# Performance work log

Hardware: AMD Instinct MI355X
Metric: run time of the kernel (lower is better)

Reference implementation:

```python
import jax, jax.numpy as jnp
import numpy as np

B, K, D = 4, 8192, 1024


def setup_inputs() -> dict:
    key = jax.random.key(0)
    kx, kw, kb = jax.random.split(key, 3)
    x = jax.random.normal(kx, (B, K, D), dtype=jnp.float32)
    # torch.nn.Linear default init: U(-1/sqrt(fan_in), 1/sqrt(fan_in))
    bound = 1.0 / np.sqrt(D)
    W = jax.random.uniform(kw, (D, D), dtype=jnp.float32, minval=-bound, maxval=bound)
    b = jax.random.uniform(kb, (D,), dtype=jnp.float32, minval=-bound, maxval=bound)
    return {"x": x, "W": W, "b": b}


def reference(x, W, b):
    # lam_t = sigmoid(x_t @ W^T + b): compute for all timesteps in one GEMM
    lam = jax.nn.sigmoid(jnp.einsum("bkd,ed->bke", x, W) + b)  # [B,K,D]
    u_gated = (1.0 - lam) * x  # [B,K,D]

    def step(s, inputs):
        lam_t, ug_t = inputs  # each [B,D]
        s = lam_t * s + ug_t
        return s, s

    s0 = jnp.zeros((x.shape[0], x.shape[2]), dtype=x.dtype)
    # scan over time axis: move K to leading dim
    _, ys = jax.lax.scan(step, s0, (jnp.swapaxes(lam, 0, 1), jnp.swapaxes(u_gated, 0, 1)))
    return jnp.swapaxes(ys, 0, 1)  # [B,K,D]
```

## Files before the change

### kernel.cpp

```cpp
#include <hip/hip_runtime.h>
#include <hip/hip_bf16.h>
#include <cstdint>
#include <cstddef>

#define B_ 4
#define K_ 8192
#define D_ 1024
#define M_ (B_*K_)

#define CCH 256
#define LCH (K_/CCH)

typedef __bf16 bf16x8 __attribute__((ext_vector_type(8)));
typedef float  f32x4  __attribute__((ext_vector_type(4)));

typedef __attribute__((address_space(1))) void as1void;
typedef __attribute__((address_space(3))) void as3void;

__device__ __forceinline__ void gload_lds16(const void* g, void* l) {
  __builtin_amdgcn_global_load_lds((as1void*)g, (as3void*)l, 16, 0, 0);
}

__device__ __forceinline__ unsigned short f2bf_rne(float f) {
  unsigned u = __builtin_bit_cast(unsigned, f);
  u += 0x7fffu + ((u >> 16) & 1u);
  return (unsigned short)(u >> 16);
}

__global__ __launch_bounds__(256) void cvt_f32_to_bf16(
    const float* __restrict__ in, unsigned short* __restrict__ out, int n4) {
  int stride = gridDim.x * blockDim.x;
  for (int i = blockIdx.x * blockDim.x + threadIdx.x; i < n4; i += stride) {
    float4 v = reinterpret_cast<const float4*>(in)[i];
    ushort4 o;
    o.x = f2bf_rne(v.x); o.y = f2bf_rne(v.y);
    o.z = f2bf_rne(v.z); o.w = f2bf_rne(v.w);
    reinterpret_cast<ushort4*>(out)[i] = o;
  }
}

__global__ __launch_bounds__(256) void gemm_bias_sigmoid(
    const unsigned short* __restrict__ A,
    const unsigned short* __restrict__ Bw,
    const float* __restrict__ bias,
    float* __restrict__ lam) {
  __shared__ __attribute__((aligned(16))) unsigned short Alds[128 * 32];
  __shared__ __attribute__((aligned(16))) unsigned short Blds[128 * 32];

  const int t    = threadIdx.x;
  const int wave = t >> 6;
  const int lane = t & 63;
  const int wr   = wave >> 1;
  const int wc   = wave & 1;
  const int m0   = blockIdx.x * 128;
  const int n0   = blockIdx.y * 128;

  f32x4 acc[4][4] = {};

  const int r0 = t >> 2;
  const int c0 = (t & 3) * 8;
  const unsigned short* gA0 = A  + (size_t)(m0 + r0)      * D_ + c0;
  const unsigned short* gA1 = A  + (size_t)(m0 + r0 + 64) * D_ + c0;
  const unsigned short* gB0 = Bw + (size_t)(n0 + r0)      * D_ + c0;
  const unsigned short* gB1 = Bw + (size_t)(n0 + r0 + 64) * D_ + c0;
  unsigned short* lA0 = Alds + (       wave * 64) * 8;
  unsigned short* lA1 = Alds + (256 +  wave * 64) * 8;
  unsigned short* lB0 = Blds + (       wave * 64) * 8;
  unsigned short* lB1 = Blds + (256 +  wave * 64) * 8;

  const int aoff = (wr * 64 + (lane & 15)) * 32 + ((lane >> 4) * 8);
  const int boff = (wc * 64 + (lane & 15)) * 32 + ((lane >> 4) * 8);

  for (int kt = 0; kt < D_; kt += 32) {
    gload_lds16(gA0 + kt, lA0);
    gload_lds16(gA1 + kt, lA1);
    gload_lds16(gB0 + kt, lB0);
    gload_lds16(gB1 + kt, lB1);
    __syncthreads();
    bf16x8 af[4], bf[4];
#pragma unroll
    for (int m = 0; m < 4; ++m)
      af[m] = *reinterpret_cast<const bf16x8*>(&Alds[aoff + m * 16 * 32]);
#pragma unroll
    for (int n = 0; n < 4; ++n)
      bf[n] = *reinterpret_cast<const bf16x8*>(&Blds[boff + n * 16 * 32]);
#pragma unroll
    for (int m = 0; m < 4; ++m)
#pragma unroll
      for (int n = 0; n < 4; ++n)
        acc[m][n] = __builtin_amdgcn_mfma_f32_16x16x32_bf16(af[m], bf[n], acc[m][n], 0, 0, 0);
    __syncthreads();
  }

  const int erow = m0 + wr * 64 + ((lane >> 4) << 2);
  const int ecol = n0 + wc * 64 + (lane & 15);
#pragma unroll
  for (int n = 0; n < 4; ++n) {
    const int col = ecol + n * 16;
    const float bv = bias[col];
#pragma unroll
    for (int m = 0; m < 4; ++m) {
#pragma unroll
      for (int r = 0; r < 4; ++r) {
        const int row = erow + m * 16 + r;
        const float z = acc[m][n][r] + bv;
        lam[(size_t)row * D_ + col] = 1.0f / (1.0f + __expf(-z));
      }
    }
  }
}

__global__ __launch_bounds__(256) void scan_pass1(
    const float* __restrict__ lam, const float* __restrict__ x,
    float* __restrict__ P, float* __restrict__ Aarr) {
  const int blk = blockIdx.x;
  const int b = blk / CCH, c = blk % CCH;
  const int d4 = threadIdx.x * 4;
  const size_t base = ((size_t)(b * K_ + c * LCH)) * D_ + d4;
  const float4* lp = reinterpret_cast<const float4*>(lam + base);
  const float4* xp = reinterpret_cast<const float4*>(x + base);
  float4 s = {0.f, 0.f, 0.f, 0.f};
  float4 p = {1.f, 1.f, 1.f, 1.f};
#pragma unroll 8
  for (int k = 0; k < LCH; ++k) {
    float4 l  = lp[k * (D_ / 4)];
    float4 xv = xp[k * (D_ / 4)];
    p.x *= l.x; p.y *= l.y; p.z *= l.z; p.w *= l.w;
    s.x = l.x * s.x + (1.f - l.x) * xv.x;
    s.y = l.y * s.y + (1.f - l.y) * xv.y;
    s.z = l.z * s.z + (1.f - l.z) * xv.z;
    s.w = l.w * s.w + (1.f - l.w) * xv.w;
  }
  const size_t o = ((size_t)(b * CCH + c)) * D_ + d4;
  *reinterpret_cast<float4*>(P + o)    = p;
  *reinterpret_cast<float4*>(Aarr + o) = s;
}

__global__ __launch_bounds__(256) void scan_pass2(
    const float* __restrict__ P, const float* __restrict__ Aarr,
    float* __restrict__ S) {
  const int g = blockIdx.x * 256 + threadIdx.x;
  const int b = g >> 10;
  const int d = g & 1023;
  float s = 0.f;
  size_t o = (size_t)(b * CCH) * D_ + d;
  for (int c = 0; c < CCH; ++c, o += D_) {
    S[o] = s;
    s = Aarr[o] + P[o] * s;
  }
}

__global__ __launch_bounds__(256) void scan_pass3(
    const float* __restrict__ lam, const float* __restrict__ x,
    const float* __restrict__ S, float* __restrict__ out) {
  const int blk = blockIdx.x;
  const int b = blk / CCH, c = blk % CCH;
  const int d4 = threadIdx.x * 4;
  float4 s = *reinterpret_cast<const float4*>(S + ((size_t)(b * CCH + c)) * D_ + d4);
  const size_t base = ((size_t)(b * K_ + c * LCH)) * D_ + d4;
  const float4* lp = reinterpret_cast<const float4*>(lam + base);
  const float4* xp = reinterpret_cast<const float4*>(x + base);
  float4* op = reinterpret_cast<float4*>(out + base);
#pragma unroll 8
  for (int k = 0; k < LCH; ++k) {
    float4 l  = lp[k * (D_ / 4)];
    float4 xv = xp[k * (D_ / 4)];
    s.x = l.x * s.x + (1.f - l.x) * xv.x;
    s.y = l.y * s.y + (1.f - l.y) * xv.y;
    s.z = l.z * s.z + (1.f - l.z) * xv.z;
    s.w = l.w * s.w + (1.f - l.w) * xv.w;
    op[k * (D_ / 4)] = s;
  }
}

extern "C" void kernel_launch(void* const* d_in, const int* in_sizes, int n_in,
                              void* d_out, int out_size, void* d_ws, size_t ws_size,
                              hipStream_t stream) {
  const float* x    = (const float*)d_in[0];
  const float* W    = (const float*)d_in[1];
  const float* bias = (const float*)d_in[2];
  float* out = (float*)d_out;

  char* ws = (char*)d_ws;
  unsigned short* xbf = (unsigned short*)ws;
  unsigned short* wbf = (unsigned short*)(ws + (size_t)M_ * D_ * 2);
  float* lam  = (float*)(ws + (size_t)M_ * D_ * 2 + (size_t)D_ * D_ * 2);
  float* P    = lam + (size_t)M_ * D_;
  float* Aarr = P   + (size_t)B_ * CCH * D_;
  float* S    = Aarr + (size_t)B_ * CCH * D_;

  cvt_f32_to_bf16<<<2048, 256, 0, stream>>>(x, xbf, M_ * D_ / 4);
  cvt_f32_to_bf16<<<512, 256, 0, stream>>>(W, wbf, D_ * D_ / 4);
  gemm_bias_sigmoid<<<dim3(M_ / 128, D_ / 128), 256, 0, stream>>>(xbf, wbf, bias, lam);
  scan_pass1<<<B_ * CCH, 256, 0, stream>>>(lam, x, P, Aarr);
  scan_pass2<<<(B_ * D_) / 256, 256, 0, stream>>>(P, Aarr, S);
  scan_pass3<<<B_ * CCH, 256, 0, stream>>>(lam, x, S, out);
}
```

Baseline: 477.5 us.

## Store sigmoid gates as fp16 and batch the carry-propagation scan loads

The GEMM epilogue now writes the gate tensor lam in half precision, and both scan passes read it as fp16 and widen to fp32. This halves the bytes for the largest intermediate, which is written once and read twice. The per-chunk carry arrays are re-laid out chunk-major so pass 2 reads coalesced across batch and feature. Pass 2 also loads eight chunks ahead before running the serial recurrence, which hides latency. The cost is fp16 rounding of lam, which the recurrence then compounds over long products of gates.

After: 438.8 us. 8.1% less time.

```diff
diff --git a/kernel.cpp b/kernel.cpp
--- a/kernel.cpp
+++ b/kernel.cpp
@@ -1,5 +1,6 @@
 #include <hip/hip_runtime.h>
 #include <hip/hip_bf16.h>
+#include <hip/hip_fp16.h>
 #include <cstdint>
 #include <cstddef>
 
@@ -7,12 +8,14 @@
 #define K_ 8192
 #define D_ 1024
 #define M_ (B_*K_)
+#define BD_ (B_*D_)
 
 #define CCH 256
 #define LCH (K_/CCH)
 
-typedef __bf16 bf16x8 __attribute__((ext_vector_type(8)));
-typedef float  f32x4  __attribute__((ext_vector_type(4)));
+typedef __bf16    bf16x8 __attribute__((ext_vector_type(8)));
+typedef float     f32x4  __attribute__((ext_vector_type(4)));
+typedef _Float16  f16x4  __attribute__((ext_vector_type(4)));
 
 typedef __attribute__((address_space(1))) void as1void;
 typedef __attribute__((address_space(3))) void as3void;
@@ -43,7 +46,7 @@
     const unsigned short* __restrict__ A,
     const unsigned short* __restrict__ Bw,
     const float* __restrict__ bias,
-    float* __restrict__ lam) {
+    _Float16* __restrict__ lamh) {
   __shared__ __attribute__((aligned(16))) unsigned short Alds[128 * 32];
   __shared__ __attribute__((aligned(16))) unsigned short Blds[128 * 32];
 
@@ -104,34 +107,35 @@
       for (int r = 0; r < 4; ++r) {
         const int row = erow + m * 16 + r;
         const float z = acc[m][n][r] + bv;
-        lam[(size_t)row * D_ + col] = 1.0f / (1.0f + __expf(-z));
+        lamh[(size_t)row * D_ + col] = (_Float16)(1.0f / (1.0f + __expf(-z)));
       }
     }
   }
 }
 
 __global__ __launch_bounds__(256) void scan_pass1(
-    const float* __restrict__ lam, const float* __restrict__ x,
+    const _Float16* __restrict__ lamh, const float* __restrict__ x,
     float* __restrict__ P, float* __restrict__ Aarr) {
   const int blk = blockIdx.x;
   const int b = blk / CCH, c = blk % CCH;
   const int d4 = threadIdx.x * 4;
   const size_t base = ((size_t)(b * K_ + c * LCH)) * D_ + d4;
-  const float4* lp = reinterpret_cast<const float4*>(lam + base);
+  const f16x4*  lp = reinterpret_cast<const f16x4*>(lamh + base);
   const float4* xp = reinterpret_cast<const float4*>(x + base);
   float4 s = {0.f, 0.f, 0.f, 0.f};
   float4 p = {1.f, 1.f, 1.f, 1.f};
 #pragma unroll 8
   for (int k = 0; k < LCH; ++k) {
-    float4 l  = lp[k * (D_ / 4)];
+    f16x4  lh = lp[k * (D_ / 4)];
     float4 xv = xp[k * (D_ / 4)];
-    p.x *= l.x; p.y *= l.y; p.z *= l.z; p.w *= l.w;
-    s.x = l.x * s.x + (1.f - l.x) * xv.x;
-    s.y = l.y * s.y + (1.f - l.y) * xv.y;
-    s.z = l.z * s.z + (1.f - l.z) * xv.z;
-    s.w = l.w * s.w + (1.f - l.w) * xv.w;
-  }
-  const size_t o = ((size_t)(b * CCH + c)) * D_ + d4;
+    float lx = (float)lh.x, ly = (float)lh.y, lz = (float)lh.z, lw = (float)lh.w;
+    p.x *= lx; p.y *= ly; p.z *= lz; p.w *= lw;
+    s.x = lx * s.x + (1.f - lx) * xv.x;
+    s.y = ly * s.y + (1.f - ly) * xv.y;
+    s.z = lz * s.z + (1.f - lz) * xv.z;
+    s.w = lw * s.w + (1.f - lw) * xv.w;
+  }
+  const size_t o = (size_t)c * BD_ + b * D_ + d4;
   *reinterpret_cast<float4*>(P + o)    = p;
   *reinterpret_cast<float4*>(Aarr + o) = s;
 }
@@ -140,35 +144,48 @@
     const float* __restrict__ P, const float* __restrict__ Aarr,
     float* __restrict__ S) {
   const int g = blockIdx.x * 256 + threadIdx.x;
-  const int b = g >> 10;
-  const int d = g & 1023;
   float s = 0.f;
-  size_t o = (size_t)(b * CCH) * D_ + d;
-  for (int c = 0; c < CCH; ++c, o += D_) {
-    S[o] = s;
-    s = Aarr[o] + P[o] * s;
+  size_t o = g;
+  for (int c0 = 0; c0 < CCH; c0 += 8) {
+    float p[8], a[8];
+#pragma unroll
+    for (int j = 0; j < 8; ++j) {
+      p[j] = P[o + (size_t)j * BD_];
+      a[j] = Aarr[o + (size_t)j * BD_];
+    }
+    float sv[8];
+#pragma unroll
+    for (int j = 0; j < 8; ++j) {
+      sv[j] = s;
+      s = fmaf(p[j], s, a[j]);
+    }
+#pragma unroll
+    for (int j = 0; j < 8; ++j)
+      S[o + (size_t)j * BD_] = sv[j];
+    o += (size_t)8 * BD_;
   }
 }
 
 __global__ __launch_bounds__(256) void scan_pass3(
-    const float* __restrict__ lam, const float* __restrict__ x,
+    const _Float16* __restrict__ lamh, const float* __restrict__ x,
     const float* __restrict__ S, float* __restrict__ out) {
   const int blk = blockIdx.x;
   const int b = blk / CCH, c = blk % CCH;
   const int d4 = threadIdx.x * 4;
-  float4 s = *reinterpret_cast<const float4*>(S + ((size_t)(b * CCH + c)) * D_ + d4);
+  float4 s = *reinterpret_cast<const float4*>(S + (size_t)c * BD_ + b * D_ + d4);
   const size_t base = ((size_t)(b * K_ + c * LCH)) * D_ + d4;
-  const float4* lp = reinterpret_cast<const float4*>(lam + base);
+  const f16x4*  lp = reinterpret_cast<const f16x4*>(lamh + base);
   const float4* xp = reinterpret_cast<const float4*>(x + base);
   float4* op = reinterpret_cast<float4*>(out + base);
 #pragma unroll 8
   for (int k = 0; k < LCH; ++k) {
-    float4 l  = lp[k * (D_ / 4)];
+    f16x4  lh = lp[k * (D_ / 4)];
     float4 xv = xp[k * (D_ / 4)];
-    s.x = l.x * s.x + (1.f - l.x) * xv.x;
-    s.y = l.y * s.y + (1.f - l.y) * xv.y;
-    s.z = l.z * s.z + (1.f - l.z) * xv.z;
-    s.w = l.w * s.w + (1.f - l.w) * xv.w;
+    float lx = (float)lh.x, ly = (float)lh.y, lz = (float)lh.z, lw = (float)lh.w;
+    s.x = lx * s.x + (1.f - lx) * xv.x;
+    s.y = ly * s.y + (1.f - ly) * xv.y;
+    s.z = lz * s.z + (1.f - lz) * xv.z;
+    s.w = lw * s.w + (1.f - lw) * xv.w;
     op[k * (D_ / 4)] = s;
   }
 }
@@ -184,15 +201,15 @@
   char* ws = (char*)d_ws;
   unsigned short* xbf = (unsigned short*)ws;
   unsigned short* wbf = (unsigned short*)(ws + (size_t)M_ * D_ * 2);
-  float* lam  = (float*)(ws + (size_t)M_ * D_ * 2 + (size_t)D_ * D_ * 2);
-  float* P    = lam + (size_t)M_ * D_;
-  float* Aarr = P   + (size_t)B_ * CCH * D_;
-  float* S    = Aarr + (size_t)B_ * CCH * D_;
+  _Float16* lamh = (_Float16*)(ws + (size_t)M_ * D_ * 2 + (size_t)D_ * D_ * 2);
+  float* P    = (float*)((char*)lamh + (size_t)M_ * D_ * 2);
+  float* Aarr = P   + (size_t)CCH * BD_;
+  float* S    = Aarr + (size_t)CCH * BD_;
 
   cvt_f32_to_bf16<<<2048, 256, 0, stream>>>(x, xbf, M_ * D_ / 4);
   cvt_f32_to_bf16<<<512, 256, 0, stream>>>(W, wbf, D_ * D_ / 4);
-  gemm_bias_sigmoid<<<dim3(M_ / 128, D_ / 128), 256, 0, stream>>>(xbf, wbf, bias, lam);
-  scan_pass1<<<B_ * CCH, 256, 0, stream>>>(lam, x, P, Aarr);
-  scan_pass2<<<(B_ * D_) / 256, 256, 0, stream>>>(P, Aarr, S);
-  scan_pass3<<<B_ * CCH, 256, 0, stream>>>(lam, x, S, out);
-}
+  gemm_bias_sigmoid<<<dim3(M_ / 128, D_ / 128), 256, 0, stream>>>(xbf, wbf, bias, lamh);
+  scan_pass1<<<B_ * CCH, 256, 0, stream>>>(lamh, x, P, Aarr);
+  scan_pass2<<<BD_ / 256, 256, 0, stream>>>(P, Aarr, S);
+  scan_pass3<<<B_ * CCH, 256, 0, stream>>>(lamh, x, S, out);
+}
```
